# Optimization experiments

Measured on AMD Instinct MI355X. Metric: run time of the kernel, lower is better.

Reference implementation:

```python
import jax, jax.numpy as jnp
import numpy as np

NUM_CLASSES = 5
VDIM = 16
IN_CH = 512
B, H, W = 32, 64, 64
LEVEL_OFFSETS = [0, 2, 5, 9]  # flat offsets of levels 1..4 (2,3,4,5 nodes)


def conv1x1(x, w, b):
    # x: [B,C,H,W], w: [O,C], b: [O] -> [B,O,H,W]
    return jnp.einsum('bchw,oc->bohw', x, w) + b[None, :, None, None]


def setup_inputs() -> dict:
    key = jax.random.key(0)
    ks = jax.random.split(key, 8)
    features = jax.random.normal(ks[0], (B, IN_CH, H, W), dtype=jnp.float32)
    # He init (fan_out = out_channels for 1x1 convs), biases zero
    root_w = jax.random.normal(ks[1], (VDIM, IN_CH), dtype=jnp.float32) * np.sqrt(2.0 / VDIM)
    root_b = jnp.zeros((VDIM,), jnp.float32)
    level_w = jax.random.normal(ks[2], (14, VDIM, VDIM), dtype=jnp.float32) * np.sqrt(2.0 / VDIM)
    level_b = jnp.zeros((14, VDIM), jnp.float32)
    m1_w = jax.random.normal(ks[3], (64, VDIM), dtype=jnp.float32) * np.sqrt(2.0 / 64.0)
    m1_b = jnp.zeros((64,), jnp.float32)
    m2_w = jax.random.normal(ks[4], (1, 64), dtype=jnp.float32) * np.sqrt(2.0 / 1.0)
    m2_b = jnp.zeros((1,), jnp.float32)
    return dict(features=features, root_w=root_w, root_b=root_b,
                level_w=level_w, level_b=level_b,
                m1_w=m1_w, m1_b=m1_b, m2_w=m2_w, m2_b=m2_b)


def reference(features, root_w, root_b, level_w, level_b, m1_w, m1_b, m2_w, m2_b):
    b = features.shape[0]
    feats = [conv1x1(features, root_w, root_b)]  # level 0: root, [B,VDIM,H,W]
    for level in range(1, NUM_CLASSES):
        off = LEVEL_OFFSETS[level - 1]
        num_nodes = level + 1
        nxt = []
        for node in range(num_nodes):
            pl = max(0, node - 1)
            pr = min(node, level - 1)
            if pl == pr:
                parent = feats[pl]
            else:
                # L2 norm of GAP-pooled parent vectors; pick larger-norm parent
                ln = jnp.linalg.norm(feats[pl].mean(axis=(2, 3)), axis=1)  # [B]
                rn = jnp.linalg.norm(feats[pr].mean(axis=(2, 3)), axis=1)
                sel = (rn > ln).astype(features.dtype)[:, None, None, None]
                parent = feats[pl] * (1.0 - sel) + feats[pr] * sel
            nxt.append(conv1x1(parent, level_w[off + node], level_b[off + node]))
        feats = nxt
    # leaves: NUM_CLASSES tensors [B,VDIM,H,W]
    leaf_pooled = jnp.stack([f.mean(axis=(2, 3)) for f in feats], axis=1)  # [B,K,VDIM]
    class_logits = jnp.linalg.norm(leaf_pooled, axis=2)                    # [B,K]
    selected_class = jnp.argmax(class_logits, axis=1)                      # [B]
    leaf_stack = jnp.stack(feats, axis=1)                                  # [B,K,VDIM,H,W]
    sel_idx = selected_class[:, None, None, None, None]
    selected_feat = jnp.take_along_axis(leaf_stack, sel_idx, axis=1)[:, 0]  # [B,VDIM,H,W]
    feat_norm = jnp.linalg.norm(selected_feat, axis=1, keepdims=True) + 1e-8
    normalized = selected_feat / feat_norm
    m1 = jax.nn.relu(conv1x1(normalized, m1_w, m1_b))
    m2 = conv1x1(m1, m2_w, m2_b)                 # [B,1,H,W]
    mantissa_raw = m2.mean(axis=(2, 3))[:, 0]    # [B]
    mantissa = jax.nn.sigmoid(mantissa_raw) * 0.75 + 0.75
    return (class_logits, mantissa, selected_class)
```

## Files before the change

kernel.cpp:

```cpp
#include <hip/hip_runtime.h>
#include <math.h>

#define HW 4096
#define NB 32
#define VD 16

#define OFF_M0P   0
#define OFF_MSP   8192
#define OFF_M     8448
#define OFF_C     16640
#define OFF_P0    17152
#define OFF_P1    2114304

__global__ __launch_bounds__(128) void k_root(const float* __restrict__ feat,
                                              const float* __restrict__ rw,
                                              const float* __restrict__ rb,
                                              float* __restrict__ pbase,
                                              float* __restrict__ m0p) {
    const int b  = blockIdx.y;
    const int s  = blockIdx.z;
    const int bx = blockIdx.x;
    const int px = bx * 512 + threadIdx.x * 4;
    const int cb = s * 256;
    const float* fp = feat + (size_t)b * 512 * HW + (size_t)cb * HW + px;

    float4 acc[VD];
#pragma unroll
    for (int o = 0; o < VD; ++o) {
        float bb = (s == 0) ? rb[o] : 0.0f;
        acc[o].x = bb; acc[o].y = bb; acc[o].z = bb; acc[o].w = bb;
    }

    for (int c = 0; c < 256; c += 4) {
        float4 f0 = *(const float4*)(fp + (size_t)(c + 0) * HW);
        float4 f1 = *(const float4*)(fp + (size_t)(c + 1) * HW);
        float4 f2 = *(const float4*)(fp + (size_t)(c + 2) * HW);
        float4 f3 = *(const float4*)(fp + (size_t)(c + 3) * HW);
#pragma unroll
        for (int o = 0; o < VD; ++o) {
            const float* wr = rw + o * 512 + cb + c;
            float w0 = wr[0], w1 = wr[1], w2 = wr[2], w3 = wr[3];
            acc[o].x += w0 * f0.x + w1 * f1.x + w2 * f2.x + w3 * f3.x;
            acc[o].y += w0 * f0.y + w1 * f1.y + w2 * f2.y + w3 * f3.y;
            acc[o].z += w0 * f0.z + w1 * f1.z + w2 * f2.z + w3 * f3.z;
            acc[o].w += w0 * f0.w + w1 * f1.w + w2 * f2.w + w3 * f3.w;
        }
    }

    float* op = pbase + (size_t)s * 2097152 + (size_t)b * VD * HW + px;
#pragma unroll
    for (int o = 0; o < VD; ++o) *(float4*)(op + (size_t)o * HW) = acc[o];

    __shared__ float red[2][VD];
    const int lane = threadIdx.x & 63, wv = threadIdx.x >> 6;
#pragma unroll
    for (int o = 0; o < VD; ++o) {
        float v = acc[o].x + acc[o].y + acc[o].z + acc[o].w;
#pragma unroll
        for (int off = 32; off > 0; off >>= 1) v += __shfl_down(v, off);
        if (lane == 0) red[wv][o] = v;
    }
    __syncthreads();
    if (threadIdx.x < VD)
        m0p[(b * 16 + s * 8 + bx) * VD + threadIdx.x] = red[0][threadIdx.x] + red[1][threadIdx.x];
}

__global__ __launch_bounds__(64) void k_tree(const float* __restrict__ lw,
                                             const float* __restrict__ lb,
                                             float* __restrict__ ws,
                                             float* __restrict__ out) {
    const int b = blockIdx.x;
    const int t = threadIdx.x;
    __shared__ float lm[15][VD];
    __shared__ float Wst[256];
    __shared__ int   path[5];
    const int Soff[5] = {0, 1, 3, 6, 10};
    const int LOFF[4] = {0, 2, 5, 9};

    if (t < VD) {
        float s = 0.f;
        for (int k = 0; k < 16; ++k) s += ws[OFF_M0P + (b * 16 + k) * VD + t];
        lm[0][t] = s * (1.0f / HW);
    }
    __syncthreads();

    for (int l = 1; l <= 4; ++l) {
        if (t < VD) {
            for (int n = 0; n <= l; ++n) {
                int pl = (n - 1 < 0) ? 0 : (n - 1);
                int pr = (n < l - 1) ? n : (l - 1);
                const float* A = lm[Soff[l - 1] + pl];
                const float* R = lm[Soff[l - 1] + pr];
                bool takeR = false;
                if (pl != pr) {
                    float ln = 0.f, rn = 0.f;
                    for (int k = 0; k < VD; ++k) { ln += A[k] * A[k]; rn += R[k] * R[k]; }
                    takeR = sqrtf(rn) > sqrtf(ln);
                }
                int widx = LOFF[l - 1] + n;
                float s = lb[widx * VD + t];
                for (int k = 0; k < VD; ++k) {
                    float pk = takeR ? R[k] : A[k];
                    s += lw[(widx * VD + t) * VD + k] * pk;
                }
                lm[Soff[l] + n][t] = s;
            }
        }
        __syncthreads();
    }

    if (t == 0) {
        float best = -1.f; int bi = 0;
        for (int n = 0; n < 5; ++n) {
            float s = 0.f;
            for (int k = 0; k < VD; ++k) { float v = lm[10 + n][k]; s += v * v; }
            float lg = sqrtf(s);
            out[b * 5 + n] = lg;
            if (lg > best) { best = lg; bi = n; }
        }
        out[192 + b] = (float)bi;
        int node = bi;
        for (int l = 4; l >= 1; --l) {
            path[l] = LOFF[l - 1] + node;
            int pl = (node - 1 < 0) ? 0 : (node - 1);
            int pr = (node < l - 1) ? node : (l - 1);
            if (pl == pr) node = pl;
            else {
                float ln = 0.f, rn = 0.f;
                for (int k = 0; k < VD; ++k) {
                    float a = lm[Soff[l - 1] + pl][k], r = lm[Soff[l - 1] + pr][k];
                    ln += a * a; rn += r * r;
                }
                node = (sqrtf(rn) > sqrtf(ln)) ? pr : pl;
            }
        }
    }
    __syncthreads();

    for (int i = t; i < 256; i += 64) Wst[i] = lw[path[1] * 256 + i];
    __syncthreads();
    float Mc[VD], cc[VD];
    if (t < VD) {
        for (int i = 0; i < VD; ++i) Mc[i] = Wst[i * VD + t];
        for (int i = 0; i < VD; ++i) cc[i] = lb[path[1] * VD + i];
    }
    for (int l = 2; l <= 4; ++l) {
        __syncthreads();
        for (int i = t; i < 256; i += 64) Wst[i] = lw[path[l] * 256 + i];
        __syncthreads();
        if (t < VD) {
            float nM[VD], nc[VD];
            for (int i = 0; i < VD; ++i) {
                float sm = 0.f, sc = 0.f;
                for (int k = 0; k < VD; ++k) {
                    float w = Wst[i * VD + k];
                    sm += w * Mc[k]; sc += w * cc[k];
                }
                nM[i] = sm; nc[i] = sc + lb[path[l] * VD + i];
            }
            for (int i = 0; i < VD; ++i) { Mc[i] = nM[i]; cc[i] = nc[i]; }
        }
    }
    if (t < VD) {
        for (int i = 0; i < VD; ++i) ws[OFF_M + b * 256 + i * VD + t] = Mc[i];
        if (t == 0) for (int i = 0; i < VD; ++i) ws[OFF_C + b * VD + i] = cc[i];
    }
}

__global__ __launch_bounds__(256) void k_final(const float* __restrict__ p0,
                                               const float* __restrict__ p1,
                                               const float* __restrict__ Mg,
                                               const float* __restrict__ Cg,
                                               const float* __restrict__ m1w,
                                               const float* __restrict__ m1b,
                                               const float* __restrict__ m2w,
                                               const float* __restrict__ m2b,
                                               float* __restrict__ msp) {
    const int b = blockIdx.y;
    const int t = threadIdx.x;
    __shared__ float sM[256], sc[VD], s1w[1024], s1b[64], s2w[64];
    sM[t] = Mg[b * 256 + t];
    for (int i = t; i < 1024; i += 256) s1w[i] = m1w[i];
    if (t < 64) { s1b[t] = m1b[t]; s2w[t] = m2w[t]; }
    if (t < VD) sc[t] = Cg[b * VD + t];
    __syncthreads();

    const size_t base = (size_t)b * VD * HW + blockIdx.x * 512 + t * 2;
    float2 f[VD];
#pragma unroll
    for (int j = 0; j < VD; ++j) {
        float2 a = *(const float2*)(p0 + base + (size_t)j * HW);
        float2 c = *(const float2*)(p1 + base + (size_t)j * HW);
        f[j].x = a.x + c.x; f[j].y = a.y + c.y;
    }

    float2 v[VD];
#pragma unroll
    for (int i = 0; i < VD; ++i) {
        float2 s; s.x = s.y = sc[i];
#pragma unroll
        for (int j = 0; j < VD; ++j) {
            float w = sM[i * VD + j];
            s.x += w * f[j].x; s.y += w * f[j].y;
        }
        v[i] = s;
    }

    float2 n2; n2.x = n2.y = 0.f;
#pragma unroll
    for (int i = 0; i < VD; ++i) { n2.x += v[i].x * v[i].x; n2.y += v[i].y * v[i].y; }
    float2 inv;
    inv.x = 1.f / (sqrtf(n2.x) + 1e-8f);
    inv.y = 1.f / (sqrtf(n2.y) + 1e-8f);
#pragma unroll
    for (int i = 0; i < VD; ++i) { v[i].x *= inv.x; v[i].y *= inv.y; }

    float mb = m2b[0];
    float2 s2; s2.x = s2.y = mb;
#pragma unroll 8
    for (int o = 0; o < 64; ++o) {
        float2 h; h.x = h.y = s1b[o];
#pragma unroll
        for (int i = 0; i < VD; ++i) {
            float w = s1w[o * VD + i];
            h.x += w * v[i].x; h.y += w * v[i].y;
        }
        h.x = fmaxf(h.x, 0.f); h.y = fmaxf(h.y, 0.f);
        float w2 = s2w[o];
        s2.x += w2 * h.x; s2.y += w2 * h.y;
    }
    float psum = s2.x + s2.y;

    const int lane = t & 63, wv = t >> 6;
#pragma unroll
    for (int off = 32; off > 0; off >>= 1) psum += __shfl_down(psum, off);
    __shared__ float rs[4];
    if (lane == 0) rs[wv] = psum;
    __syncthreads();
    if (t == 0) msp[b * 8 + blockIdx.x] = rs[0] + rs[1] + rs[2] + rs[3];
}

__global__ __launch_bounds__(64) void k_mant(const float* __restrict__ msp,
                                             float* __restrict__ out) {
    int b = threadIdx.x;
    if (b < NB) {
        float m = 0.f;
        for (int k = 0; k < 8; ++k) m += msp[b * 8 + k];
        m *= (1.0f / HW);
        out[160 + b] = (1.0f / (1.0f + expf(-m))) * 0.75f + 0.75f;
    }
}

extern "C" void kernel_launch(void* const* d_in, const int* in_sizes, int n_in,
                              void* d_out, int out_size, void* d_ws, size_t ws_size,
                              hipStream_t stream) {
    const float* feat    = (const float*)d_in[0];
    const float* root_w  = (const float*)d_in[1];
    const float* root_b  = (const float*)d_in[2];
    const float* level_w = (const float*)d_in[3];
    const float* level_b = (const float*)d_in[4];
    const float* m1w     = (const float*)d_in[5];
    const float* m1b     = (const float*)d_in[6];
    const float* m2w     = (const float*)d_in[7];
    const float* m2b     = (const float*)d_in[8];
    float* ws  = (float*)d_ws;
    float* out = (float*)d_out;

    k_root<<<dim3(8, NB, 2), 128, 0, stream>>>(feat, root_w, root_b,
                                               ws + OFF_P0, ws + OFF_M0P);
    k_tree<<<NB, 64, 0, stream>>>(level_w, level_b, ws, out);
    k_final<<<dim3(8, NB), 256, 0, stream>>>(ws + OFF_P0, ws + OFF_P1,
                                             ws + OFF_M, ws + OFF_C,
                                             m1w, m1b, m2w, m2b, ws + OFF_MSP);
    k_mant<<<1, 64, 0, stream>>>(ws + OFF_MSP, out);
}
```

Baseline: 494.3 us.

## Split root conv into four channel chunks with transposed weights and prefetch

The root 1x1 conv now splits its 512 input channels into four chunks of 128 instead of two, with 256-thread blocks covering 1024 pixels. Root weights are pre-transposed by a new small kernel so each channel's 16 outputs sit contiguously, and feature loads are software-prefetched one step ahead. The final kernel then sums four partial outputs instead of two. This raises parallelism and load overlap in the bandwidth-bound root pass, at the cost of an extra launch and twice the partial-sum traffic written and then read back.

Measured after the change: 417.6 us. 1.18x faster.

```diff
diff --git a/kernel.cpp b/kernel.cpp
--- a/kernel.cpp
+++ b/kernel.cpp
@@ -4,25 +4,38 @@
 #define HW 4096
 #define NB 32
 #define VD 16
+#define CPB 128
 
 #define OFF_M0P   0
 #define OFF_MSP   8192
 #define OFF_M     8448
 #define OFF_C     16640
-#define OFF_P0    17152
-#define OFF_P1    2114304
-
-__global__ __launch_bounds__(128) void k_root(const float* __restrict__ feat,
-                                              const float* __restrict__ rw,
+#define OFF_WT    17152
+#define OFF_P     25344
+#define PSZ       2097152
+
+__global__ __launch_bounds__(256) void k_trans(const float* __restrict__ rw,
+                                               float* __restrict__ wt) {
+    int i = blockIdx.x * 256 + threadIdx.x;
+    if (i < 512 * VD) {
+        int c = i >> 4, o = i & 15;
+        wt[i] = rw[o * 512 + c];
+    }
+}
+
+__global__ __launch_bounds__(256) void k_root(const float* __restrict__ feat,
+                                              const float* __restrict__ wt,
                                               const float* __restrict__ rb,
                                               float* __restrict__ pbase,
                                               float* __restrict__ m0p) {
     const int b  = blockIdx.y;
     const int s  = blockIdx.z;
     const int bx = blockIdx.x;
-    const int px = bx * 512 + threadIdx.x * 4;
-    const int cb = s * 256;
-    const float* fp = feat + (size_t)b * 512 * HW + (size_t)cb * HW + px;
+    const int t  = threadIdx.x;
+    const int px = bx * 1024 + t * 4;
+    const int cb = s * CPB;
+    const float* fp = feat + ((size_t)b * 512 + cb) * HW + px;
+    const float* wp = wt + (size_t)cb * VD;
 
     float4 acc[VD];
 #pragma unroll
@@ -31,28 +44,38 @@
         acc[o].x = bb; acc[o].y = bb; acc[o].z = bb; acc[o].w = bb;
     }
 
-    for (int c = 0; c < 256; c += 4) {
-        float4 f0 = *(const float4*)(fp + (size_t)(c + 0) * HW);
-        float4 f1 = *(const float4*)(fp + (size_t)(c + 1) * HW);
-        float4 f2 = *(const float4*)(fp + (size_t)(c + 2) * HW);
-        float4 f3 = *(const float4*)(fp + (size_t)(c + 3) * HW);
-#pragma unroll
-        for (int o = 0; o < VD; ++o) {
-            const float* wr = rw + o * 512 + cb + c;
-            float w0 = wr[0], w1 = wr[1], w2 = wr[2], w3 = wr[3];
-            acc[o].x += w0 * f0.x + w1 * f1.x + w2 * f2.x + w3 * f3.x;
-            acc[o].y += w0 * f0.y + w1 * f1.y + w2 * f2.y + w3 * f3.y;
-            acc[o].z += w0 * f0.z + w1 * f1.z + w2 * f2.z + w3 * f3.z;
-            acc[o].w += w0 * f0.w + w1 * f1.w + w2 * f2.w + w3 * f3.w;
-        }
-    }
-
-    float* op = pbase + (size_t)s * 2097152 + (size_t)b * VD * HW + px;
+    float4 cur[4], nxt[4];
+#pragma unroll
+    for (int k = 0; k < 4; ++k) cur[k] = *(const float4*)(fp + (size_t)k * HW);
+
+    for (int c = 0; c < CPB; c += 4) {
+        if (c + 4 < CPB) {
+#pragma unroll
+            for (int k = 0; k < 4; ++k)
+                nxt[k] = *(const float4*)(fp + (size_t)(c + 4 + k) * HW);
+        }
+        const float* wr = wp + c * VD;
+#pragma unroll
+        for (int j = 0; j < 4; ++j) {
+#pragma unroll
+            for (int o = 0; o < VD; ++o) {
+                float w = wr[j * VD + o];
+                acc[o].x += w * cur[j].x;
+                acc[o].y += w * cur[j].y;
+                acc[o].z += w * cur[j].z;
+                acc[o].w += w * cur[j].w;
+            }
+        }
+#pragma unroll
+        for (int k = 0; k < 4; ++k) cur[k] = nxt[k];
+    }
+
+    float* op = pbase + (size_t)s * PSZ + (size_t)b * VD * HW + px;
 #pragma unroll
     for (int o = 0; o < VD; ++o) *(float4*)(op + (size_t)o * HW) = acc[o];
 
-    __shared__ float red[2][VD];
-    const int lane = threadIdx.x & 63, wv = threadIdx.x >> 6;
+    __shared__ float red[4][VD];
+    const int lane = t & 63, wv = t >> 6;
 #pragma unroll
     for (int o = 0; o < VD; ++o) {
         float v = acc[o].x + acc[o].y + acc[o].z + acc[o].w;
@@ -61,8 +84,9 @@
         if (lane == 0) red[wv][o] = v;
     }
     __syncthreads();
-    if (threadIdx.x < VD)
-        m0p[(b * 16 + s * 8 + bx) * VD + threadIdx.x] = red[0][threadIdx.x] + red[1][threadIdx.x];
+    if (t < VD)
+        m0p[((b * 4 + s) * 4 + bx) * VD + t] =
+            red[0][t] + red[1][t] + red[2][t] + red[3][t];
 }
 
 __global__ __launch_bounds__(64) void k_tree(const float* __restrict__ lw,
@@ -167,8 +191,7 @@
     }
 }
 
-__global__ __launch_bounds__(256) void k_final(const float* __restrict__ p0,
-                                               const float* __restrict__ p1,
+__global__ __launch_bounds__(256) void k_final(const float* __restrict__ pbase,
                                                const float* __restrict__ Mg,
                                                const float* __restrict__ Cg,
                                                const float* __restrict__ m1w,
@@ -189,9 +212,12 @@
     float2 f[VD];
 #pragma unroll
     for (int j = 0; j < VD; ++j) {
-        float2 a = *(const float2*)(p0 + base + (size_t)j * HW);
-        float2 c = *(const float2*)(p1 + base + (size_t)j * HW);
-        f[j].x = a.x + c.x; f[j].y = a.y + c.y;
+        float2 a0 = *(const float2*)(pbase + base + (size_t)j * HW);
+        float2 a1 = *(const float2*)(pbase + PSZ + base + (size_t)j * HW);
+        float2 a2 = *(const float2*)(pbase + 2 * PSZ + base + (size_t)j * HW);
+        float2 a3 = *(const float2*)(pbase + 3 * (size_t)PSZ + base + (size_t)j * HW);
+        f[j].x = a0.x + a1.x + a2.x + a3.x;
+        f[j].y = a0.y + a1.y + a2.y + a3.y;
     }
 
     float2 v[VD];
@@ -266,11 +292,11 @@
     float* ws  = (float*)d_ws;
     float* out = (float*)d_out;
 
-    k_root<<<dim3(8, NB, 2), 128, 0, stream>>>(feat, root_w, root_b,
-                                               ws + OFF_P0, ws + OFF_M0P);
+    k_trans<<<32, 256, 0, stream>>>(root_w, ws + OFF_WT);
+    k_root<<<dim3(4, NB, 4), 256, 0, stream>>>(feat, ws + OFF_WT, root_b,
+                                               ws + OFF_P, ws + OFF_M0P);
     k_tree<<<NB, 64, 0, stream>>>(level_w, level_b, ws, out);
-    k_final<<<dim3(8, NB), 256, 0, stream>>>(ws + OFF_P0, ws + OFF_P1,
-                                             ws + OFF_M, ws + OFF_C,
+    k_final<<<dim3(8, NB), 256, 0, stream>>>(ws + OFF_P, ws + OFF_M, ws + OFF_C,
                                              m1w, m1b, m2w, m2b, ws + OFF_MSP);
     k_mant<<<1, 64, 0, stream>>>(ws + OFF_MSP, out);
 }
```
